# Kernel optimization log

Measured on AMD Instinct MI355X. Metric: run time of the kernel, lower is better.

## Reference

```python
import jax, jax.numpy as jnp
import numpy as np

B, C, H, W = 16, 64, 64, 64  # z_e shape; C == embedding_dim
K = 1024                     # num_embeddings
COMMITMENT_COST = 0.25
EPS = 1e-5


def setup_inputs() -> dict:
    key = jax.random.key(0)
    k1, k2 = jax.random.split(key)
    z_e = jax.random.normal(k1, (B, C, H, W), dtype=jnp.float32)
    # codebook init ~ U(-1/D, 1/D) as in the torch module
    emb_w = jax.random.uniform(k2, (K, C), dtype=jnp.float32, minval=-1.0 / C, maxval=1.0 / C)
    return {"z_e": z_e, "emb_w": emb_w}


def reference(z_e, emb_w):
    orig_dtype = z_e.dtype
    b, c, h, w = z_e.shape
    z = z_e.astype(jnp.float32)
    # per-channel std over (batch, h, w); computed under no_grad in torch -> stop_gradient
    std = jax.lax.stop_gradient(
        jnp.clip(jnp.std(z, axis=(0, 2, 3), keepdims=True, ddof=1), EPS, None)
    )
    z = z / std                                        # [b,c,h,w]
    zf = z.transpose(0, 2, 3, 1).reshape(-1, c)        # [N, c]
    ew = emb_w.astype(jnp.float32)                     # [K, c]
    # squared euclidean distances: ||z||^2 - 2 z.e + ||e||^2  -> [N, K]
    d = (
        jnp.sum(zf * zf, axis=1, keepdims=True)
        - 2.0 * (zf @ ew.T)
        + jnp.sum(ew * ew, axis=1)
    )
    idx = jnp.argmin(d, axis=1)                        # [N]
    z_q = ew[idx].reshape(b, h, w, c).transpose(0, 3, 1, 2)  # [b,c,h,w]
    z_sg = jax.lax.stop_gradient(z)
    commitment = COMMITMENT_COST * jnp.mean((z_sg - z_q) ** 2)
    codebook = jnp.mean((z_sg - z_q) ** 2)             # eval-mode codebook loss
    vq_loss = commitment + codebook
    z_q_st = (z + jax.lax.stop_gradient(z_q - z)).astype(orig_dtype)
    n_tokens = idx.shape[0]
    counts = jnp.zeros((K,), dtype=jnp.float32).at[idx].add(1.0)
    avg_probs = counts / n_tokens
    perplexity = jnp.exp(-jnp.sum(avg_probs * jnp.log(jnp.clip(avg_probs, 1e-10, None))))
    indices = idx.reshape(b, h, w)
    return z_q_st, vq_loss, perplexity, indices
```

## Files before the change

kernel.cpp:

```cpp
#include <hip/hip_runtime.h>
#include <math.h>
#include <float.h>

#define HW 4096
#define CHW 262144
#define NTOK 65536
#define NELEM 4194304

#define WS_LOSS 0
#define WS_STD  512
#define WS_EE   576
#define WS_ETG  1600
#define WS_HIST 67136

__global__ __launch_bounds__(1024) void k_std(const float* __restrict__ z,
                                              float* __restrict__ stdv) {
  int c = blockIdx.x;
  int tid = threadIdx.x;
  double s = 0.0, s2 = 0.0;
  const float* base = z + c * HW;
  #pragma unroll 4
  for (int jj = 0; jj < 16; ++jj) {
    int f = tid + (jj << 10);
    int b = f >> 10, off4 = f & 1023;
    float4 v = *(const float4*)(base + (size_t)b * CHW + (off4 << 2));
    s  += (double)v.x + (double)v.y + (double)v.z + (double)v.w;
    s2 += (double)v.x * v.x + (double)v.y * v.y + (double)v.z * v.z + (double)v.w * v.w;
  }
  for (int o = 32; o > 0; o >>= 1) {
    s += __shfl_down(s, o, 64);
    s2 += __shfl_down(s2, o, 64);
  }
  __shared__ double rs[16], rs2[16];
  int wv = tid >> 6, ln = tid & 63;
  if (ln == 0) { rs[wv] = s; rs2[wv] = s2; }
  __syncthreads();
  if (tid == 0) {
    double S = 0.0, S2 = 0.0;
    #pragma unroll
    for (int w = 0; w < 16; ++w) { S += rs[w]; S2 += rs2[w]; }
    const double N = (double)NTOK;
    double var = (S2 - S * S / N) / (N - 1.0);
    float sd = (float)sqrt(var);
    stdv[c] = fmaxf(sd, 1e-5f);
  }
}

__global__ __launch_bounds__(256) void k_tr(const float* __restrict__ emb,
                                            float* __restrict__ etg,
                                            float* __restrict__ eeg) {
  __shared__ float T[64][65];
  int tid = threadIdx.x;
  int k0 = blockIdx.x << 6;
  #pragma unroll
  for (int jj = 0; jj < 4; ++jj) {
    int f = tid + (jj << 8);
    int code = f >> 4, c4 = f & 15;
    float4 v = *(const float4*)(emb + (size_t)((k0 + code) << 6) + (c4 << 2));
    T[code][(c4 << 2) + 0] = v.x;
    T[code][(c4 << 2) + 1] = v.y;
    T[code][(c4 << 2) + 2] = v.z;
    T[code][(c4 << 2) + 3] = v.w;
  }
  __syncthreads();
  #pragma unroll
  for (int jj = 0; jj < 4; ++jj) {
    int f = tid + (jj << 8);
    int c = f >> 4, k4 = f & 15;
    float4 v = make_float4(T[(k4 << 2) + 0][c], T[(k4 << 2) + 1][c],
                           T[(k4 << 2) + 2][c], T[(k4 << 2) + 3][c]);
    *(float4*)(etg + c * 1024 + k0 + (k4 << 2)) = v;
  }
  if (tid < 64) {
    const float* er = emb + (size_t)((k0 + tid) << 6);
    float s = 0.f;
    #pragma unroll
    for (int c = 0; c < 64; ++c) s = fmaf(er[c], er[c], s);
    eeg[k0 + tid] = s;
  }
}

__global__ __launch_bounds__(256, 2) void k_vq(
    const float* __restrict__ z_e, const float* __restrict__ emb,
    const float* __restrict__ stdv, const float* __restrict__ eeg,
    const float* __restrict__ etg,
    float* __restrict__ out_zq, float* __restrict__ out_idx,
    float* __restrict__ loss_part) {
  __shared__ float zt[64 * 128];
  __shared__ float et[64 * 128];
  __shared__ float eet[128];
  __shared__ float zzt[128];
  __shared__ float sstd[64];
  __shared__ float rbd[2 * 128];
  __shared__ int   rbk[2 * 128];
  __shared__ int   skf[128];
  __shared__ float sred[4];

  int tid = threadIdx.x;
  int lane = tid & 63;
  int wv = tid >> 6;
  int blk = blockIdx.x;
  int b = blk >> 5;
  int s0 = (blk & 31) << 7;

  if (tid < 64) sstd[tid] = stdv[tid];
  __syncthreads();

  const float* zbase = z_e + (size_t)b * CHW + s0;
  float4 pf[8];
  float eet0 = 0.f;
  #pragma unroll
  for (int jj = 0; jj < 8; ++jj) {
    int f = tid + (jj << 8);
    int c = f >> 5, t4 = f & 31;
    float4 v = *(const float4*)(zbase + (size_t)c * HW + (t4 << 2));
    float sd = sstd[c];
    v.x /= sd; v.y /= sd; v.z /= sd; v.w /= sd;
    *(float4*)&zt[(c << 7) + (t4 << 2)] = v;
  }
  #pragma unroll
  for (int jj = 0; jj < 8; ++jj) {
    int f = tid + (jj << 8);
    int c = f >> 5, k4 = f & 31;
    pf[jj] = *(const float4*)(etg + c * 1024 + (k4 << 2));
  }
  if (tid < 128) eet0 = eeg[tid];
  __syncthreads();

  if (tid < 128) {
    float a = 0.f;
    #pragma unroll
    for (int c = 0; c < 64; ++c) { float v = zt[(c << 7) + tid]; a = fmaf(v, v, a); }
    zzt[tid] = a;
    eet[tid] = eet0;
  }
  #pragma unroll
  for (int jj = 0; jj < 8; ++jj) {
    int f = tid + (jj << 8);
    int c = f >> 5, k4 = f & 31;
    *(float4*)&et[(c << 7) + (k4 << 2)] = pf[jj];
  }
  __syncthreads();

  int i8 = (lane >> 3) << 3;
  int j8 = (lane & 7) << 3;
  int wt = wv >> 1, wc = wv & 1;
  int toff = wt * 64 + i8;
  int koff = wc * 64 + j8;

  float zzr[8];
  #pragma unroll
  for (int ii = 0; ii < 8; ++ii) zzr[ii] = zzt[toff + ii];

  float bd[8]; int bk[8];
  #pragma unroll
  for (int ii = 0; ii < 8; ++ii) { bd[ii] = FLT_MAX; bk[ii] = 0; }

  const float4* ztp = (const float4*)&zt[toff];
  const float4* etp = (const float4*)&et[koff];

  for (int tile = 0; tile < 8; ++tile) {
    float eer[8];
    #pragma unroll
    for (int jj = 0; jj < 8; ++jj) eer[jj] = eet[koff + jj];

    float4 npf[8]; float neet = 0.f;
    if (tile < 7) {
      const float* src = etg + ((tile + 1) << 7);
      #pragma unroll
      for (int jj = 0; jj < 8; ++jj) {
        int f = tid + (jj << 8);
        int c = f >> 5, k4 = f & 31;
        npf[jj] = *(const float4*)(src + c * 1024 + (k4 << 2));
      }
      if (tid < 128) neet = eeg[((tile + 1) << 7) + tid];
    }

    float2 acc[8][4];
    #pragma unroll
    for (int ii = 0; ii < 8; ++ii)
      #pragma unroll
      for (int jj = 0; jj < 4; ++jj) acc[ii][jj] = make_float2(0.f, 0.f);

    #pragma unroll 8
    for (int c = 0; c < 64; ++c) {
      float4 za = ztp[c << 5], zb4 = ztp[(c << 5) + 1];
      float4 ea = etp[c << 5], eb4 = etp[(c << 5) + 1];
      float zv[8] = {za.x, za.y, za.z, za.w, zb4.x, zb4.y, zb4.z, zb4.w};
      float ev[8] = {ea.x, ea.y, ea.z, ea.w, eb4.x, eb4.y, eb4.z, eb4.w};
      #pragma unroll
      for (int ii = 0; ii < 8; ++ii) {
        float z1 = zv[ii];
        #pragma unroll
        for (int jj = 0; jj < 4; ++jj) {
          acc[ii][jj].x = fmaf(z1, ev[2 * jj], acc[ii][jj].x);
          acc[ii][jj].y = fmaf(z1, ev[2 * jj + 1], acc[ii][jj].y);
        }
      }
    }

    int kb = (tile << 7) + koff;
    #pragma unroll
    for (int ii = 0; ii < 8; ++ii) {
      float z2 = zzr[ii];
      #pragma unroll
      for (int jj = 0; jj < 4; ++jj) {
        float dd0 = (z2 - 2.0f * acc[ii][jj].x) + eer[2 * jj];
        float dd1 = (z2 - 2.0f * acc[ii][jj].y) + eer[2 * jj + 1];
        if (dd0 < bd[ii]) { bd[ii] = dd0; bk[ii] = kb + 2 * jj; }
        if (dd1 < bd[ii]) { bd[ii] = dd1; bk[ii] = kb + 2 * jj + 1; }
      }
    }

    __syncthreads();
    if (tile < 7) {
      #pragma unroll
      for (int jj = 0; jj < 8; ++jj) {
        int f = tid + (jj << 8);
        int c = f >> 5, k4 = f & 31;
        *(float4*)&et[(c << 7) + (k4 << 2)] = npf[jj];
      }
      if (tid < 128) eet[tid] = neet;
      __syncthreads();
    }
  }

  #pragma unroll
  for (int m = 1; m <= 4; m <<= 1) {
    #pragma unroll
    for (int ii = 0; ii < 8; ++ii) {
      float od = __shfl_xor(bd[ii], m, 64);
      int   ok = __shfl_xor(bk[ii], m, 64);
      if (od < bd[ii] || (od == bd[ii] && ok < bk[ii])) { bd[ii] = od; bk[ii] = ok; }
    }
  }
  if ((lane & 7) == 0) {
    #pragma unroll
    for (int ii = 0; ii < 8; ++ii) {
      rbd[wc * 128 + toff + ii] = bd[ii];
      rbk[wc * 128 + toff + ii] = bk[ii];
    }
  }
  __syncthreads();

  if (tid < 128) {
    float d0 = rbd[tid];       int k0 = rbk[tid];
    float d1 = rbd[128 + tid]; int k1 = rbk[128 + tid];
    int kb2 = (d1 < d0 || (d1 == d0 && k1 < k0)) ? k1 : k0;
    skf[tid] = kb2;
    out_idx[(blk << 7) + tid] = (float)kb2;
  }
  __syncthreads();

  int t = tid & 127;
  int ch = tid >> 7;
  int kq = skf[t];
  const float* eq = emb + (size_t)(kq << 6) + (ch << 5);
  float lsum = 0.f;
  float* ob = out_zq + (size_t)b * CHW + s0 + t;
  #pragma unroll
  for (int jj = 0; jj < 32; ++jj) {
    int c = (ch << 5) + jj;
    float zv = zt[(c << 7) + t];
    float e = eq[jj];
    float df = zv - e;
    lsum = fmaf(df, df, lsum);
    ob[(size_t)c * HW] = zv + (e - zv);
  }
  for (int o = 32; o > 0; o >>= 1) lsum += __shfl_down(lsum, o, 64);
  if (lane == 0) sred[wv] = lsum;
  __syncthreads();
  if (tid == 0) loss_part[blk] = sred[0] + sred[1] + sred[2] + sred[3];
}

__global__ __launch_bounds__(256) void k_hist(const float* __restrict__ out_idx,
                                              int* __restrict__ histg) {
  __shared__ int hist[1024];
  int tid = threadIdx.x;
  int blk = blockIdx.x;
  #pragma unroll
  for (int jj = 0; jj < 4; ++jj) hist[tid + (jj << 8)] = 0;
  __syncthreads();
  const float2* idx2 = (const float2*)(out_idx + (blk << 12));
  #pragma unroll
  for (int jj = 0; jj < 8; ++jj) {
    float2 v = idx2[tid + (jj << 8)];
    atomicAdd(&hist[(int)v.x], 1);
    atomicAdd(&hist[(int)v.y], 1);
  }
  __syncthreads();
  #pragma unroll
  for (int jj = 0; jj < 4; ++jj) {
    int i = tid + (jj << 8);
    histg[(blk << 10) + i] = hist[i];
  }
}

__global__ __launch_bounds__(1024) void k_fin(const float* __restrict__ loss_part,
                                              const int* __restrict__ histg,
                                              float* __restrict__ out_scalars) {
  int tid = threadIdx.x;
  int cnt = 0;
  #pragma unroll
  for (int bI = 0; bI < 16; ++bI) cnt += histg[(bI << 10) + tid];
  double ls = 0.0;
  if (tid < 512) ls = (double)loss_part[tid];
  float p = (float)cnt * (1.0f / 65536.0f);
  float lg = logf(fmaxf(p, 1e-10f));
  double hs = (double)(p * lg);
  for (int o = 32; o > 0; o >>= 1) {
    ls += __shfl_down(ls, o, 64);
    hs += __shfl_down(hs, o, 64);
  }
  __shared__ double rl[16], rh[16];
  int wv = tid >> 6, ln = tid & 63;
  if (ln == 0) { rl[wv] = ls; rh[wv] = hs; }
  __syncthreads();
  if (tid == 0) {
    double L = 0.0, Hn = 0.0;
    #pragma unroll
    for (int w = 0; w < 16; ++w) { L += rl[w]; Hn += rh[w]; }
    float m = (float)(L / (double)NELEM);
    out_scalars[0] = 0.25f * m + m;
    out_scalars[1] = expf((float)(-Hn));
  }
}

extern "C" void kernel_launch(void* const* d_in, const int* in_sizes, int n_in,
                              void* d_out, int out_size, void* d_ws, size_t ws_size,
                              hipStream_t stream) {
  const float* z_e = (const float*)d_in[0];
  const float* emb = (const float*)d_in[1];
  float* ws = (float*)d_ws;
  float* loss_part = ws + WS_LOSS;
  float* stdv = ws + WS_STD;
  float* eeg = ws + WS_EE;
  float* etg = ws + WS_ETG;
  int* histg = (int*)(ws + WS_HIST);

  float* out = (float*)d_out;
  float* out_zq = out;
  float* out_scalars = out + NELEM;
  float* out_idx = out + NELEM + 2;

  k_std<<<64, 1024, 0, stream>>>(z_e, stdv);
  k_tr<<<16, 256, 0, stream>>>(emb, etg, eeg);
  k_vq<<<512, 256, 0, stream>>>(z_e, emb, stdv, eeg, etg, out_zq, out_idx, loss_part);
  k_hist<<<16, 256, 0, stream>>>(out_idx, histg);
  k_fin<<<1, 1024, 0, stream>>>(loss_part, histg, out_scalars);
}
```

Before: 209.5 us.

## Shrink VQ codebook tile, add direct global-to-LDS loads, fuse pre/post kernels

The distance kernel now uses 64-code tiles and an 8x4 per-thread microtile, so it needs half the accumulator registers. Launch bounds rise to 3 blocks per CU, and codebook tiles are copied with global_load_lds builtins instead of a register-staged prefetch. The std and codebook-transpose kernels merge into one launch, and the histogram and finalize kernels merge into one single-block launch. In exchange, the explicit prefetch overlap is gone, each tile now costs two barriers, LDS reads per FMA rise, and the whole histogram runs on one block.

```diff
diff --git a/kernel.cpp b/kernel.cpp
--- a/kernel.cpp
+++ b/kernel.cpp
@@ -11,84 +11,92 @@
 #define WS_STD  512
 #define WS_EE   576
 #define WS_ETG  1600
-#define WS_HIST 67136
-
-__global__ __launch_bounds__(1024) void k_std(const float* __restrict__ z,
-                                              float* __restrict__ stdv) {
-  int c = blockIdx.x;
-  int tid = threadIdx.x;
-  double s = 0.0, s2 = 0.0;
-  const float* base = z + c * HW;
-  #pragma unroll 4
-  for (int jj = 0; jj < 16; ++jj) {
-    int f = tid + (jj << 10);
-    int b = f >> 10, off4 = f & 1023;
-    float4 v = *(const float4*)(base + (size_t)b * CHW + (off4 << 2));
-    s  += (double)v.x + (double)v.y + (double)v.z + (double)v.w;
-    s2 += (double)v.x * v.x + (double)v.y * v.y + (double)v.z * v.z + (double)v.w * v.w;
-  }
-  for (int o = 32; o > 0; o >>= 1) {
-    s += __shfl_down(s, o, 64);
-    s2 += __shfl_down(s2, o, 64);
-  }
+
+__device__ __forceinline__ void gload_lds16(const float* g, float* l) {
+  __builtin_amdgcn_global_load_lds(
+      (const __attribute__((address_space(1))) unsigned int*)g,
+      (__attribute__((address_space(3))) unsigned int*)l, 16, 0, 0);
+}
+
+__global__ __launch_bounds__(1024) void k_pre(const float* __restrict__ z,
+                                              const float* __restrict__ emb,
+                                              float* __restrict__ stdv,
+                                              float* __restrict__ etg,
+                                              float* __restrict__ eeg) {
   __shared__ double rs[16], rs2[16];
-  int wv = tid >> 6, ln = tid & 63;
-  if (ln == 0) { rs[wv] = s; rs2[wv] = s2; }
-  __syncthreads();
-  if (tid == 0) {
-    double S = 0.0, S2 = 0.0;
-    #pragma unroll
-    for (int w = 0; w < 16; ++w) { S += rs[w]; S2 += rs2[w]; }
-    const double N = (double)NTOK;
-    double var = (S2 - S * S / N) / (N - 1.0);
-    float sd = (float)sqrt(var);
-    stdv[c] = fmaxf(sd, 1e-5f);
-  }
-}
-
-__global__ __launch_bounds__(256) void k_tr(const float* __restrict__ emb,
-                                            float* __restrict__ etg,
-                                            float* __restrict__ eeg) {
   __shared__ float T[64][65];
   int tid = threadIdx.x;
-  int k0 = blockIdx.x << 6;
-  #pragma unroll
-  for (int jj = 0; jj < 4; ++jj) {
-    int f = tid + (jj << 8);
-    int code = f >> 4, c4 = f & 15;
-    float4 v = *(const float4*)(emb + (size_t)((k0 + code) << 6) + (c4 << 2));
-    T[code][(c4 << 2) + 0] = v.x;
-    T[code][(c4 << 2) + 1] = v.y;
-    T[code][(c4 << 2) + 2] = v.z;
-    T[code][(c4 << 2) + 3] = v.w;
-  }
-  __syncthreads();
-  #pragma unroll
-  for (int jj = 0; jj < 4; ++jj) {
-    int f = tid + (jj << 8);
-    int c = f >> 4, k4 = f & 15;
-    float4 v = make_float4(T[(k4 << 2) + 0][c], T[(k4 << 2) + 1][c],
-                           T[(k4 << 2) + 2][c], T[(k4 << 2) + 3][c]);
-    *(float4*)(etg + c * 1024 + k0 + (k4 << 2)) = v;
-  }
-  if (tid < 64) {
-    const float* er = emb + (size_t)((k0 + tid) << 6);
-    float s = 0.f;
-    #pragma unroll
-    for (int c = 0; c < 64; ++c) s = fmaf(er[c], er[c], s);
-    eeg[k0 + tid] = s;
-  }
-}
-
-__global__ __launch_bounds__(256, 2) void k_vq(
+  int blk = blockIdx.x;
+  if (blk < 64) {
+    int c = blk;
+    double s = 0.0, s2 = 0.0;
+    const float* base = z + c * HW;
+    #pragma unroll 4
+    for (int jj = 0; jj < 16; ++jj) {
+      int f = tid + (jj << 10);
+      int b = f >> 10, off4 = f & 1023;
+      float4 v = *(const float4*)(base + (size_t)b * CHW + (off4 << 2));
+      s  += (double)v.x + (double)v.y + (double)v.z + (double)v.w;
+      s2 += (double)v.x * v.x + (double)v.y * v.y + (double)v.z * v.z + (double)v.w * v.w;
+    }
+    for (int o = 32; o > 0; o >>= 1) {
+      s += __shfl_down(s, o, 64);
+      s2 += __shfl_down(s2, o, 64);
+    }
+    int wv = tid >> 6, ln = tid & 63;
+    if (ln == 0) { rs[wv] = s; rs2[wv] = s2; }
+    __syncthreads();
+    if (tid == 0) {
+      double S = 0.0, S2 = 0.0;
+      #pragma unroll
+      for (int w = 0; w < 16; ++w) { S += rs[w]; S2 += rs2[w]; }
+      const double N = (double)NTOK;
+      double var = (S2 - S * S / N) / (N - 1.0);
+      float sd = (float)sqrt(var);
+      stdv[c] = fmaxf(sd, 1e-5f);
+    }
+  } else {
+    int k0 = (blk - 64) << 6;
+    {
+      int code = tid >> 4, c4 = tid & 15;
+      float4 v = *(const float4*)(emb + (size_t)((k0 + code) << 6) + (c4 << 2));
+      T[code][(c4 << 2) + 0] = v.x;
+      T[code][(c4 << 2) + 1] = v.y;
+      T[code][(c4 << 2) + 2] = v.z;
+      T[code][(c4 << 2) + 3] = v.w;
+    }
+    __syncthreads();
+    {
+      int c = tid >> 4, k4 = tid & 15;
+      float4 v = make_float4(T[(k4 << 2) + 0][c], T[(k4 << 2) + 1][c],
+                             T[(k4 << 2) + 2][c], T[(k4 << 2) + 3][c]);
+      *(float4*)(etg + c * 1024 + k0 + (k4 << 2)) = v;
+    }
+    if (tid < 64) {
+      const float* er = emb + (size_t)((k0 + tid) << 6);
+      float s = 0.f;
+      #pragma unroll
+      for (int c = 0; c < 64; ++c) s = fmaf(er[c], er[c], s);
+      eeg[k0 + tid] = s;
+    }
+  }
+}
+
+#define FMA8(ii, zc) \
+  acc[ii].x = fmaf(zc, ea.x, acc[ii].x); \
+  acc[ii].y = fmaf(zc, ea.y, acc[ii].y); \
+  acc[ii].z = fmaf(zc, ea.z, acc[ii].z); \
+  acc[ii].w = fmaf(zc, ea.w, acc[ii].w);
+
+__global__ __launch_bounds__(256, 3) void k_vq(
     const float* __restrict__ z_e, const float* __restrict__ emb,
     const float* __restrict__ stdv, const float* __restrict__ eeg,
     const float* __restrict__ etg,
     float* __restrict__ out_zq, float* __restrict__ out_idx,
     float* __restrict__ loss_part) {
   __shared__ float zt[64 * 128];
-  __shared__ float et[64 * 128];
-  __shared__ float eet[128];
+  __shared__ float et[64 * 64];
+  __shared__ float eetS[64];
   __shared__ float zzt[128];
   __shared__ float sstd[64];
   __shared__ float rbd[2 * 128];
@@ -107,8 +115,6 @@
   __syncthreads();
 
   const float* zbase = z_e + (size_t)b * CHW + s0;
-  float4 pf[8];
-  float eet0 = 0.f;
   #pragma unroll
   for (int jj = 0; jj < 8; ++jj) {
     int f = tid + (jj << 8);
@@ -118,13 +124,6 @@
     v.x /= sd; v.y /= sd; v.z /= sd; v.w /= sd;
     *(float4*)&zt[(c << 7) + (t4 << 2)] = v;
   }
-  #pragma unroll
-  for (int jj = 0; jj < 8; ++jj) {
-    int f = tid + (jj << 8);
-    int c = f >> 5, k4 = f & 31;
-    pf[jj] = *(const float4*)(etg + c * 1024 + (k4 << 2));
-  }
-  if (tid < 128) eet0 = eeg[tid];
   __syncthreads();
 
   if (tid < 128) {
@@ -132,21 +131,13 @@
     #pragma unroll
     for (int c = 0; c < 64; ++c) { float v = zt[(c << 7) + tid]; a = fmaf(v, v, a); }
     zzt[tid] = a;
-    eet[tid] = eet0;
-  }
-  #pragma unroll
-  for (int jj = 0; jj < 8; ++jj) {
-    int f = tid + (jj << 8);
-    int c = f >> 5, k4 = f & 31;
-    *(float4*)&et[(c << 7) + (k4 << 2)] = pf[jj];
-  }
-  __syncthreads();
-
-  int i8 = (lane >> 3) << 3;
-  int j8 = (lane & 7) << 3;
-  int wt = wv >> 1, wc = wv & 1;
-  int toff = wt * 64 + i8;
-  int koff = wc * 64 + j8;
+  }
+  __syncthreads();
+
+  int toff = ((wv >> 1) << 6) + ((lane >> 3) << 3);
+  int kloc = ((wv & 1) << 5) + ((lane & 7) << 2);
+  int tq4 = toff >> 2;
+  int kq4 = kloc >> 2;
 
   float zzr[8];
   #pragma unroll
@@ -156,72 +147,49 @@
   #pragma unroll
   for (int ii = 0; ii < 8; ++ii) { bd[ii] = FLT_MAX; bk[ii] = 0; }
 
-  const float4* ztp = (const float4*)&zt[toff];
-  const float4* etp = (const float4*)&et[koff];
-
-  for (int tile = 0; tile < 8; ++tile) {
-    float eer[8];
-    #pragma unroll
-    for (int jj = 0; jj < 8; ++jj) eer[jj] = eet[koff + jj];
-
-    float4 npf[8]; float neet = 0.f;
-    if (tile < 7) {
-      const float* src = etg + ((tile + 1) << 7);
+  int c0 = tid >> 4;
+  int k16 = (tid & 15) << 2;
+  const float* gbase = etg + c0 * 1024 + k16;
+  float* lbase = et + (c0 << 6) + k16;
+
+  for (int tile = 0; tile < 16; ++tile) {
+    __syncthreads();
+    {
+      const float* gsrc = gbase + (tile << 6);
       #pragma unroll
-      for (int jj = 0; jj < 8; ++jj) {
-        int f = tid + (jj << 8);
-        int c = f >> 5, k4 = f & 31;
-        npf[jj] = *(const float4*)(src + c * 1024 + (k4 << 2));
-      }
-      if (tid < 128) neet = eeg[((tile + 1) << 7) + tid];
-    }
-
-    float2 acc[8][4];
-    #pragma unroll
-    for (int ii = 0; ii < 8; ++ii)
-      #pragma unroll
-      for (int jj = 0; jj < 4; ++jj) acc[ii][jj] = make_float2(0.f, 0.f);
+      for (int jj = 0; jj < 4; ++jj)
+        gload_lds16(gsrc + jj * 16384, lbase + jj * 1024);
+      if (tid < 64) eetS[tid] = eeg[(tile << 6) + tid];
+    }
+    __syncthreads();
+
+    float4 acc[8];
+    #pragma unroll
+    for (int ii = 0; ii < 8; ++ii) acc[ii] = make_float4(0.f, 0.f, 0.f, 0.f);
 
     #pragma unroll 8
     for (int c = 0; c < 64; ++c) {
-      float4 za = ztp[c << 5], zb4 = ztp[(c << 5) + 1];
-      float4 ea = etp[c << 5], eb4 = etp[(c << 5) + 1];
-      float zv[8] = {za.x, za.y, za.z, za.w, zb4.x, zb4.y, zb4.z, zb4.w};
-      float ev[8] = {ea.x, ea.y, ea.z, ea.w, eb4.x, eb4.y, eb4.z, eb4.w};
-      #pragma unroll
-      for (int ii = 0; ii < 8; ++ii) {
-        float z1 = zv[ii];
-        #pragma unroll
-        for (int jj = 0; jj < 4; ++jj) {
-          acc[ii][jj].x = fmaf(z1, ev[2 * jj], acc[ii][jj].x);
-          acc[ii][jj].y = fmaf(z1, ev[2 * jj + 1], acc[ii][jj].y);
-        }
-      }
-    }
-
-    int kb = (tile << 7) + koff;
+      float4 ea = ((const float4*)et)[(c << 4) + kq4];
+      float4 za = ((const float4*)zt)[(c << 5) + tq4];
+      float4 zb = ((const float4*)zt)[(c << 5) + tq4 + 1];
+      FMA8(0, za.x) FMA8(1, za.y) FMA8(2, za.z) FMA8(3, za.w)
+      FMA8(4, zb.x) FMA8(5, zb.y) FMA8(6, zb.z) FMA8(7, zb.w)
+    }
+
+    int kb = (tile << 6) + kloc;
+    float e0 = eetS[kloc], e1 = eetS[kloc + 1];
+    float e2 = eetS[kloc + 2], e3 = eetS[kloc + 3];
     #pragma unroll
     for (int ii = 0; ii < 8; ++ii) {
       float z2 = zzr[ii];
-      #pragma unroll
-      for (int jj = 0; jj < 4; ++jj) {
-        float dd0 = (z2 - 2.0f * acc[ii][jj].x) + eer[2 * jj];
-        float dd1 = (z2 - 2.0f * acc[ii][jj].y) + eer[2 * jj + 1];
-        if (dd0 < bd[ii]) { bd[ii] = dd0; bk[ii] = kb + 2 * jj; }
-        if (dd1 < bd[ii]) { bd[ii] = dd1; bk[ii] = kb + 2 * jj + 1; }
-      }
-    }
-
-    __syncthreads();
-    if (tile < 7) {
-      #pragma unroll
-      for (int jj = 0; jj < 8; ++jj) {
-        int f = tid + (jj << 8);
-        int c = f >> 5, k4 = f & 31;
-        *(float4*)&et[(c << 7) + (k4 << 2)] = npf[jj];
-      }
-      if (tid < 128) eet[tid] = neet;
-      __syncthreads();
+      float dd0 = (z2 - 2.0f * acc[ii].x) + e0;
+      float dd1 = (z2 - 2.0f * acc[ii].y) + e1;
+      float dd2 = (z2 - 2.0f * acc[ii].z) + e2;
+      float dd3 = (z2 - 2.0f * acc[ii].w) + e3;
+      if (dd0 < bd[ii]) { bd[ii] = dd0; bk[ii] = kb; }
+      if (dd1 < bd[ii]) { bd[ii] = dd1; bk[ii] = kb + 1; }
+      if (dd2 < bd[ii]) { bd[ii] = dd2; bk[ii] = kb + 2; }
+      if (dd3 < bd[ii]) { bd[ii] = dd3; bk[ii] = kb + 3; }
     }
   }
 
@@ -235,11 +203,9 @@
     }
   }
   if ((lane & 7) == 0) {
-    #pragma unroll
-    for (int ii = 0; ii < 8; ++ii) {
-      rbd[wc * 128 + toff + ii] = bd[ii];
-      rbk[wc * 128 + toff + ii] = bk[ii];
-    }
+    int base = ((wv & 1) << 7) + toff;
+    #pragma unroll
+    for (int ii = 0; ii < 8; ++ii) { rbd[base + ii] = bd[ii]; rbk[base + ii] = bk[ii]; }
   }
   __syncthreads();
 
@@ -273,46 +239,31 @@
   if (tid == 0) loss_part[blk] = sred[0] + sred[1] + sred[2] + sred[3];
 }
 
-__global__ __launch_bounds__(256) void k_hist(const float* __restrict__ out_idx,
-                                              int* __restrict__ histg) {
+__global__ __launch_bounds__(1024) void k_post(const float* __restrict__ loss_part,
+                                               const float* __restrict__ out_idx,
+                                               float* __restrict__ out_scalars) {
   __shared__ int hist[1024];
+  __shared__ double rl[16], rh[16];
   int tid = threadIdx.x;
-  int blk = blockIdx.x;
-  #pragma unroll
-  for (int jj = 0; jj < 4; ++jj) hist[tid + (jj << 8)] = 0;
-  __syncthreads();
-  const float2* idx2 = (const float2*)(out_idx + (blk << 12));
-  #pragma unroll
-  for (int jj = 0; jj < 8; ++jj) {
-    float2 v = idx2[tid + (jj << 8)];
+  hist[tid] = 0;
+  __syncthreads();
+  const float2* idx2 = (const float2*)out_idx;
+  #pragma unroll
+  for (int jj = 0; jj < 32; ++jj) {
+    float2 v = idx2[tid + (jj << 10)];
     atomicAdd(&hist[(int)v.x], 1);
     atomicAdd(&hist[(int)v.y], 1);
   }
   __syncthreads();
-  #pragma unroll
-  for (int jj = 0; jj < 4; ++jj) {
-    int i = tid + (jj << 8);
-    histg[(blk << 10) + i] = hist[i];
-  }
-}
-
-__global__ __launch_bounds__(1024) void k_fin(const float* __restrict__ loss_part,
-                                              const int* __restrict__ histg,
-                                              float* __restrict__ out_scalars) {
-  int tid = threadIdx.x;
-  int cnt = 0;
-  #pragma unroll
-  for (int bI = 0; bI < 16; ++bI) cnt += histg[(bI << 10) + tid];
   double ls = 0.0;
   if (tid < 512) ls = (double)loss_part[tid];
-  float p = (float)cnt * (1.0f / 65536.0f);
+  float p = (float)hist[tid] * (1.0f / 65536.0f);
   float lg = logf(fmaxf(p, 1e-10f));
   double hs = (double)(p * lg);
   for (int o = 32; o > 0; o >>= 1) {
     ls += __shfl_down(ls, o, 64);
     hs += __shfl_down(hs, o, 64);
   }
-  __shared__ double rl[16], rh[16];
   int wv = tid >> 6, ln = tid & 63;
   if (ln == 0) { rl[wv] = ls; rh[wv] = hs; }
   __syncthreads();
@@ -336,16 +287,13 @@
   float* stdv = ws + WS_STD;
   float* eeg = ws + WS_EE;
   float* etg = ws + WS_ETG;
-  int* histg = (int*)(ws + WS_HIST);
 
   float* out = (float*)d_out;
   float* out_zq = out;
   float* out_scalars = out + NELEM;
   float* out_idx = out + NELEM + 2;
 
-  k_std<<<64, 1024, 0, stream>>>(z_e, stdv);
-  k_tr<<<16, 256, 0, stream>>>(emb, etg, eeg);
+  k_pre<<<80, 1024, 0, stream>>>(z_e, emb, stdv, etg, eeg);
   k_vq<<<512, 256, 0, stream>>>(z_e, emb, stdv, eeg, etg, out_zq, out_idx, loss_part);
-  k_hist<<<16, 256, 0, stream>>>(out_idx, histg);
-  k_fin<<<1, 1024, 0, stream>>>(loss_part, histg, out_scalars);
-}
+  k_post<<<1, 1024, 0, stream>>>(loss_part, out_idx, out_scalars);
+}
```

Result: no change. 206.6 us (-1.4%).
